# Kernel tuning notes

Measured on AMD Instinct MI355X. Metric: run time of the kernel, lower is better.

The kernel has to match this reference:

```python
import jax, jax.numpy as jnp
import numpy as np

VOCAB = 50000
EMBED = 256
LABELS = 2
DEPTH = 10          # complete binary tree: 2**DEPTH leaves
B = 256             # batch of trees
L = 2 ** DEPTH      # leaves per tree


def setup_inputs() -> dict:
    key = jax.random.key(0)
    ks = jax.random.split(key, 7)
    token_ids = jax.random.randint(ks[0], (B, L), 0, VOCAB)
    labels = jax.random.randint(ks[1], (B,), 0, LABELS)
    emb = jax.random.normal(ks[2], (VOCAB, EMBED), dtype=jnp.float32)
    W_w = jax.random.normal(ks[3], (EMBED, 2 * EMBED), dtype=jnp.float32) * (1.0 / np.sqrt(2 * EMBED))
    W_b = jax.random.normal(ks[4], (EMBED,), dtype=jnp.float32) * 0.01
    P_w = jax.random.normal(ks[5], (LABELS, EMBED), dtype=jnp.float32) * (1.0 / np.sqrt(EMBED))
    P_b = jax.random.normal(ks[6], (LABELS,), dtype=jnp.float32) * 0.01
    return {"token_ids": token_ids, "labels": labels, "emb": emb,
            "W_w": W_w, "W_b": W_b, "P_w": P_w, "P_b": P_b}


def reference(token_ids, labels, emb, W_w, W_b, P_w, P_b):
    # Leaves: relu(embedding(token))  -> [B, L, E]
    x = jax.nn.relu(emb[token_ids])
    # Level-by-level combine: currentNode = relu(W @ cat(left, right) + b)
    # Leaf order is left-to-right, so adjacent pairs (2k, 2k+1) are siblings;
    # reshape concatenates (left, right) along features, matching torch.cat((l, r), 1).
    while x.shape[1] > 1:
        bsz, n, e = x.shape
        lr = x.reshape(bsz, n // 2, 2 * e)                       # [B, n/2, 2E]
        x = jax.nn.relu(jnp.einsum('bnf,ef->bne', lr, W_w) + W_b)
    root = x[:, 0]                                               # [B, E]
    logits = root @ P_w.T + P_b                                  # [B, label_size]
    prediction = jnp.argmax(logits, axis=1)
    logp = jax.nn.log_softmax(logits, axis=-1)
    loss = -jnp.take_along_axis(logp, labels[:, None], axis=1)[:, 0]  # per-tree CE
    return prediction, loss
```

## Files before the change

### kernel.cpp

```cpp
#include <hip/hip_runtime.h>
#include <hip/hip_bf16.h>
#include <math.h>

#define EMBED   256
#define KDIM    512
#define BATCH   256
#define BM      128

typedef float  f32x4   __attribute__((ext_vector_type(4)));
typedef __bf16 bf16x8  __attribute__((ext_vector_type(8)));
typedef unsigned short ushort8 __attribute__((ext_vector_type(8)));

__device__ __forceinline__ unsigned short f2h(float f) {
    unsigned int u = __float_as_uint(f);
    u += 0x7FFFu + ((u >> 16) & 1u);
    return (unsigned short)(u >> 16);
}
__device__ __forceinline__ float h2f(unsigned short h) {
    return __uint_as_float(((unsigned int)h) << 16);
}
__device__ __forceinline__ void gload16(const void* g, void* l) {
    __builtin_amdgcn_global_load_lds(
        (const __attribute__((address_space(1))) unsigned int*)g,
        (__attribute__((address_space(3))) unsigned int*)l, 16, 0, 0);
}

template<int LV1, int WPREP>
__global__ __launch_bounds__(1024, 4) void gemm_tree(
    const unsigned short* __restrict__ Xh, const unsigned short* __restrict__ Xl,
    const unsigned short* __restrict__ Wh, const unsigned short* __restrict__ Wl,
    const float*  __restrict__ Wf,
    const float*  __restrict__ bias,
    unsigned short* __restrict__ Yh, unsigned short* __restrict__ Yl,
    const int* __restrict__ tok, const float* __restrict__ emb)
{
    __shared__ __align__(16) unsigned short AhL[2][4096], AlL[2][4096];
    __shared__ __align__(16) unsigned short BhL[2][8192], BlL[2][8192];

    const int tid = threadIdx.x;
    const int wid = tid >> 6;
    const int l   = tid & 63;
    const int q   = l >> 4;
    const int rr  = l & 15;
    const int m0  = blockIdx.x * BM;
    const int waveM = wid >> 2;
    const int waveN = wid & 3;

    int tokA0 = 0, tokA1 = 0;
    if constexpr (LV1) {
        if (wid < 8) {
            const int r = m0 + wid * 16 + rr;
            tokA0 = tok[2 * r];
            tokA1 = tok[2 * r + 1];
        }
    }

    float va[8];
    float vb[8];

    f32x4 acc[2][4] = {};

    auto stage_issue = [&](int buf, int k0) {
        const int joff = k0 >> 8;
        const int c    = (k0 & 255) + q * 8;
        if constexpr (LV1) {
            if (wid < 8) {
                const int t = joff ? tokA1 : tokA0;
                const float* e = emb + (size_t)t * EMBED + c;
                *(float4*)&va[0] = *(const float4*)e;
                *(float4*)&va[4] = *(const float4*)(e + 4);
            }
            if constexpr (WPREP) {
                #pragma unroll
                for (int j = 0; j < 2; ++j) {
                    const int sb = wid * 2 + j;
                    const int s  = sb & 15;
                    const size_t off = (size_t)(s * 16 + rr) * KDIM + k0 + q * 8;
                    if (sb < 16) gload16(Wh + off, &BhL[buf][s * 512]);
                    else         gload16(Wl + off, &BlL[buf][s * 512]);
                }
            } else {
                const float* ws = Wf + (size_t)(wid * 16 + rr) * KDIM + k0 + q * 8;
                *(float4*)&vb[0] = *(const float4*)ws;
                *(float4*)&vb[4] = *(const float4*)(ws + 4);
            }
        } else {
            if constexpr (WPREP) {
                #pragma unroll
                for (int j = 0; j < 3; ++j) {
                    const int slot = wid * 3 + j;
                    if (slot < 16) {
                        const int s = slot & 7;
                        const size_t off = (size_t)(2 * (m0 + s * 16 + rr) + joff) * EMBED + c;
                        if (slot < 8) gload16(Xh + off, &AhL[buf][s * 512]);
                        else          gload16(Xl + off, &AlL[buf][s * 512]);
                    } else {
                        const int s = slot & 15;
                        const size_t off = (size_t)(s * 16 + rr) * KDIM + k0 + q * 8;
                        if (slot < 32) gload16(Wh + off, &BhL[buf][s * 512]);
                        else           gload16(Wl + off, &BlL[buf][s * 512]);
                    }
                }
            } else {
                const int s = wid & 7;
                const size_t off = (size_t)(2 * (m0 + s * 16 + rr) + joff) * EMBED + c;
                if (wid < 8) gload16(Xh + off, &AhL[buf][s * 512]);
                else         gload16(Xl + off, &AlL[buf][s * 512]);
                const float* ws = Wf + (size_t)(wid * 16 + rr) * KDIM + k0 + q * 8;
                *(float4*)&vb[0] = *(const float4*)ws;
                *(float4*)&vb[4] = *(const float4*)(ws + 4);
            }
        }
    };

    auto stage_finish = [&](int buf) {
        if constexpr (LV1) {
            if (wid < 8) {
                ushort8 hs, ls;
                #pragma unroll
                for (int i = 0; i < 8; ++i) {
                    const float f = fmaxf(va[i], 0.f);
                    const unsigned short h = f2h(f);
                    hs[i] = h;
                    ls[i] = f2h(f - h2f(h));
                }
                *(ushort8*)&AhL[buf][wid * 512 + l * 8] = hs;
                *(ushort8*)&AlL[buf][wid * 512 + l * 8] = ls;
            }
        }
        if constexpr (!WPREP) {
            ushort8 hs, ls;
            #pragma unroll
            for (int i = 0; i < 8; ++i) {
                const unsigned short h = f2h(vb[i]);
                hs[i] = h;
                ls[i] = f2h(vb[i] - h2f(h));
            }
            *(ushort8*)&BhL[buf][wid * 512 + l * 8] = hs;
            *(ushort8*)&BlL[buf][wid * 512 + l * 8] = ls;
        }
    };

    stage_issue(0, 0);
    stage_finish(0);
    __syncthreads();

    for (int t = 0; t < 16; ++t) {
        const int cur = t & 1;
        const int nxt = cur ^ 1;
        if (t < 15) stage_issue(nxt, (t + 1) << 5);

        bf16x8 ah[2], al[2], bh[4], bl[4];
        #pragma unroll
        for (int mi = 0; mi < 2; ++mi) {
            ah[mi] = *(const bf16x8*)&AhL[cur][(waveM * 2 + mi) * 512 + l * 8];
            al[mi] = *(const bf16x8*)&AlL[cur][(waveM * 2 + mi) * 512 + l * 8];
        }
        #pragma unroll
        for (int ni = 0; ni < 4; ++ni) {
            bh[ni] = *(const bf16x8*)&BhL[cur][(waveN * 4 + ni) * 512 + l * 8];
            bl[ni] = *(const bf16x8*)&BlL[cur][(waveN * 4 + ni) * 512 + l * 8];
        }
        #pragma unroll
        for (int mi = 0; mi < 2; ++mi)
            #pragma unroll
            for (int ni = 0; ni < 4; ++ni)
                acc[mi][ni] = __builtin_amdgcn_mfma_f32_16x16x32_bf16(ah[mi], bh[ni], acc[mi][ni], 0, 0, 0);
        #pragma unroll
        for (int mi = 0; mi < 2; ++mi)
            #pragma unroll
            for (int ni = 0; ni < 4; ++ni)
                acc[mi][ni] = __builtin_amdgcn_mfma_f32_16x16x32_bf16(al[mi], bh[ni], acc[mi][ni], 0, 0, 0);
        #pragma unroll
        for (int mi = 0; mi < 2; ++mi)
            #pragma unroll
            for (int ni = 0; ni < 4; ++ni)
                acc[mi][ni] = __builtin_amdgcn_mfma_f32_16x16x32_bf16(ah[mi], bl[ni], acc[mi][ni], 0, 0, 0);

        if (t < 15) stage_finish(nxt);
        __syncthreads();
    }

    #pragma unroll
    for (int ni = 0; ni < 4; ++ni) {
        const int col = waveN * 64 + ni * 16 + rr;
        const float bv = bias[col];
        #pragma unroll
        for (int mi = 0; mi < 2; ++mi) {
            const int row0 = m0 + waveM * 32 + mi * 16 + q * 4;
            #pragma unroll
            for (int jj = 0; jj < 4; ++jj) {
                const float y = fmaxf(acc[mi][ni][jj] + bv, 0.f);
                const unsigned short h = f2h(y);
                Yh[(size_t)(row0 + jj) * EMBED + col] = h;
                Yl[(size_t)(row0 + jj) * EMBED + col] = f2h(y - h2f(h));
            }
        }
    }
}

template<int WPREP>
__global__ __launch_bounds__(256) void tail_kernel(
    const unsigned short* __restrict__ Xh5, const unsigned short* __restrict__ Xl5,
    const unsigned short* __restrict__ Wh, const unsigned short* __restrict__ Wl,
    const float* __restrict__ Wf, const float* __restrict__ bias,
    const float* __restrict__ Pw, const float* __restrict__ Pb,
    const int* __restrict__ labels, float* __restrict__ out)
{
    __shared__ __align__(16) unsigned short X0h[8192], X0l[8192];
    __shared__ __align__(16) unsigned short X1h[4096], X1l[4096];
    __shared__ __align__(16) unsigned short BhT[2][8192], BlT[2][8192];

    const int tid = threadIdx.x;
    const int w   = tid >> 6;
    const int l   = tid & 63;
    const int q   = l >> 4;
    const int rr  = l & 15;
    const int b   = blockIdx.x;

    {
        const int row = tid >> 3;
        const int c0  = (tid & 7) * 32;
        #pragma unroll
        for (int i = 0; i < 4; ++i) {
            const int col = c0 + i * 8;
            const int sw  = (row * 256 + col) ^ ((row & 7) << 3);
            *(ushort8*)&X0h[sw] = *(const ushort8*)&Xh5[(size_t)(b * 32 + row) * EMBED + col];
            *(ushort8*)&X0l[sw] = *(const ushort8*)&Xl5[(size_t)(b * 32 + row) * EMBED + col];
        }
    }

    auto stageB = [&](int buf, int k0) {
        if constexpr (WPREP) {
            #pragma unroll
            for (int j = 0; j < 8; ++j) {
                const int sb = w * 8 + j;
                const int s  = sb & 15;
                const size_t off = (size_t)(s * 16 + rr) * KDIM + k0 + q * 8;
                if (sb < 16) gload16(Wh + off, &BhT[buf][s * 512]);
                else         gload16(Wl + off, &BlT[buf][s * 512]);
            }
        } else {
            #pragma unroll
            for (int j = 0; j < 4; ++j) {
                const int u = w * 4 + j;
                const float* ws = Wf + (size_t)(u * 16 + rr) * KDIM + k0 + q * 8;
                float v[8];
                *(float4*)&v[0] = *(const float4*)ws;
                *(float4*)&v[4] = *(const float4*)(ws + 4);
                ushort8 hs, ls;
                #pragma unroll
                for (int i = 0; i < 8; ++i) {
                    const unsigned short h = f2h(v[i]);
                    hs[i] = h;
                    ls[i] = f2h(v[i] - h2f(h));
                }
                *(ushort8*)&BhT[buf][u * 512 + l * 8] = hs;
                *(ushort8*)&BlT[buf][u * 512 + l * 8] = ls;
            }
        }
    };

    float bv[4];
    #pragma unroll
    for (int ni = 0; ni < 4; ++ni) bv[ni] = bias[w * 64 + ni * 16 + rr];

    stageB(0, 0);
    __syncthreads();

    int g = 0;
    for (int lv = 0; lv < 5; ++lv) {
        unsigned short* srch = (lv & 1) ? X1h : X0h;
        unsigned short* srcl = (lv & 1) ? X1l : X0l;
        unsigned short* dsth = (lv & 1) ? X0h : X1h;
        unsigned short* dstl = (lv & 1) ? X0l : X1l;
        const int Mout = 16 >> lv;

        f32x4 acc[4] = {};
        for (int t = 0; t < 16; ++t, ++g) {
            const int cur = g & 1;
            if (g < 79) stageB(cur ^ 1, ((t + 1) & 15) * 32);

            const int k0   = t * 32;
            const int joff = k0 >> 8;
            const int c    = (k0 & 255) + q * 8;
            const int row  = 2 * rr + joff;
            const int idx  = (row * 256 + c) ^ ((row & 7) << 3);
            const bf16x8 a_h = *(const bf16x8*)&srch[idx];
            const bf16x8 a_l = *(const bf16x8*)&srcl[idx];

            bf16x8 bh4[4], bl4[4];
            #pragma unroll
            for (int ni = 0; ni < 4; ++ni) {
                bh4[ni] = *(const bf16x8*)&BhT[cur][(w * 4 + ni) * 512 + l * 8];
                bl4[ni] = *(const bf16x8*)&BlT[cur][(w * 4 + ni) * 512 + l * 8];
            }
            #pragma unroll
            for (int ni = 0; ni < 4; ++ni)
                acc[ni] = __builtin_amdgcn_mfma_f32_16x16x32_bf16(a_h, bh4[ni], acc[ni], 0, 0, 0);
            #pragma unroll
            for (int ni = 0; ni < 4; ++ni)
                acc[ni] = __builtin_amdgcn_mfma_f32_16x16x32_bf16(a_l, bh4[ni], acc[ni], 0, 0, 0);
            #pragma unroll
            for (int ni = 0; ni < 4; ++ni)
                acc[ni] = __builtin_amdgcn_mfma_f32_16x16x32_bf16(a_h, bl4[ni], acc[ni], 0, 0, 0);

            __syncthreads();
        }

        #pragma unroll
        for (int ni = 0; ni < 4; ++ni) {
            const int col = w * 64 + ni * 16 + rr;
            #pragma unroll
            for (int jj = 0; jj < 4; ++jj) {
                const int row = q * 4 + jj;
                if (row < Mout) {
                    const float y = fmaxf(acc[ni][jj] + bv[ni], 0.f);
                    const unsigned short h = f2h(y);
                    const int idx = (row * 256 + col) ^ ((row & 7) << 3);
                    dsth[idx] = h;
                    dstl[idx] = f2h(y - h2f(h));
                }
            }
        }
        __syncthreads();
    }

    if (w == 0) {
        float s0 = 0.f, s1 = 0.f;
        #pragma unroll
        for (int i = 0; i < 4; ++i) {
            const int col = l + i * 64;
            const float x = h2f(X1h[col]) + h2f(X1l[col]);
            s0 = fmaf(x, Pw[col], s0);
            s1 = fmaf(x, Pw[EMBED + col], s1);
        }
        #pragma unroll
        for (int off = 32; off > 0; off >>= 1) {
            s0 += __shfl_down(s0, off);
            s1 += __shfl_down(s1, off);
        }
        if (l == 0) {
            const float l0 = s0 + Pb[0];
            const float l1 = s1 + Pb[1];
            const int pred = (l1 > l0) ? 1 : 0;
            const float m  = fmaxf(l0, l1);
            const float lse = m + logf(expf(l0 - m) + expf(l1 - m));
            const int lab = labels[b];
            out[b]         = (float)pred;
            out[BATCH + b] = lse - (lab ? l1 : l0);
        }
    }
}

__global__ __launch_bounds__(256) void prep_w(const float* __restrict__ W,
                                              unsigned short* __restrict__ Wh,
                                              unsigned short* __restrict__ Wl)
{
    const int i = blockIdx.x * 256 + threadIdx.x;
    const float w = W[i];
    const unsigned short h = f2h(w);
    Wh[i] = h;
    Wl[i] = f2h(w - h2f(h));
}

extern "C" void kernel_launch(void* const* d_in, const int* in_sizes, int n_in,
                              void* d_out, int out_size, void* d_ws, size_t ws_size,
                              hipStream_t stream)
{
    const int*   token_ids = (const int*)d_in[0];
    const int*   labels    = (const int*)d_in[1];
    const float* emb       = (const float*)d_in[2];
    const float* W_w       = (const float*)d_in[3];
    const float* W_b       = (const float*)d_in[4];
    const float* P_w       = (const float*)d_in[5];
    const float* P_b       = (const float*)d_in[6];
    float*       out       = (float*)d_out;

    unsigned short* Ah_buf = (unsigned short*)d_ws;
    unsigned short* Al_buf = Ah_buf + (size_t)131072 * 256;
    unsigned short* Bh_buf = Al_buf + (size_t)131072 * 256;
    unsigned short* Bl_buf = Bh_buf + (size_t)65536 * 256;
    unsigned short* Wh     = Bl_buf + (size_t)65536 * 256;
    unsigned short* Wl     = Wh + 131072;

    const size_t need_wprep = ((size_t)131072 * 256 * 2 + (size_t)65536 * 256 * 2 + 2 * 131072) * 2;
    const bool wprep = ws_size >= need_wprep;

    if (wprep) prep_w<<<512, 256, 0, stream>>>(W_w, Wh, Wl);

    int R = 131072;
    const unsigned short *inh = nullptr, *inl = nullptr;
    for (int lv = 1; lv <= 5; ++lv) {
        unsigned short* yh = (lv & 1) ? Ah_buf : Bh_buf;
        unsigned short* yl = (lv & 1) ? Al_buf : Bl_buf;
        dim3 grid(R / BM);
        if (lv == 1) {
            if (wprep) gemm_tree<1,1><<<grid, 1024, 0, stream>>>(nullptr, nullptr, Wh, Wl, W_w, W_b, yh, yl, token_ids, emb);
            else       gemm_tree<1,0><<<grid, 1024, 0, stream>>>(nullptr, nullptr, Wh, Wl, W_w, W_b, yh, yl, token_ids, emb);
        } else {
            if (wprep) gemm_tree<0,1><<<grid, 1024, 0, stream>>>(inh, inl, Wh, Wl, W_w, W_b, yh, yl, nullptr, nullptr);
            else       gemm_tree<0,0><<<grid, 1024, 0, stream>>>(inh, inl, Wh, Wl, W_w, W_b, yh, yl, nullptr, nullptr);
        }
        inh = yh; inl = yl; R >>= 1;
    }

    if (wprep) tail_kernel<1><<<BATCH, 256, 0, stream>>>(inh, inl, Wh, Wl, W_w, W_b, P_w, P_b, labels, out);
    else       tail_kernel<0><<<BATCH, 256, 0, stream>>>(inh, inl, Wh, Wl, W_w, W_b, P_w, P_b, labels, out);
}
```

Before: 434.8 us.

## Retile tree GEMM to 128x128 tiles with 4 waves and swizzled grid

Replaces the 1024-thread block computing a 128x256 tile with a 256-thread block computing a 128x128 tile. Each wave now holds a 64x64 accumulator, which raises MFMA work per LDS read. The grid doubles along N and block order is swizzled so tiles sharing an A slab run near each other. The double-buffered prefetch is dropped for a single buffer with two barriers per K step. That lowers LDS use and may raise occupancy, but load latency is no longer hidden behind compute within a block.

```diff
diff --git a/kernel.cpp b/kernel.cpp
--- a/kernel.cpp
+++ b/kernel.cpp
@@ -6,6 +6,7 @@
 #define KDIM    512
 #define BATCH   256
 #define BM      128
+#define BN      128
 
 typedef float  f32x4   __attribute__((ext_vector_type(4)));
 typedef __bf16 bf16x8  __attribute__((ext_vector_type(8)));
@@ -26,7 +27,7 @@
 }
 
 template<int LV1, int WPREP>
-__global__ __launch_bounds__(1024, 4) void gemm_tree(
+__global__ __launch_bounds__(256) void gemm_tree(
     const unsigned short* __restrict__ Xh, const unsigned short* __restrict__ Xl,
     const unsigned short* __restrict__ Wh, const unsigned short* __restrict__ Wl,
     const float*  __restrict__ Wf,
@@ -34,160 +35,137 @@
     unsigned short* __restrict__ Yh, unsigned short* __restrict__ Yl,
     const int* __restrict__ tok, const float* __restrict__ emb)
 {
-    __shared__ __align__(16) unsigned short AhL[2][4096], AlL[2][4096];
-    __shared__ __align__(16) unsigned short BhL[2][8192], BlL[2][8192];
+    __shared__ __align__(16) unsigned short AhL[4096], AlL[4096];
+    __shared__ __align__(16) unsigned short BhL[4096], BlL[4096];
 
     const int tid = threadIdx.x;
-    const int wid = tid >> 6;
+    const int w   = tid >> 6;
     const int l   = tid & 63;
     const int q   = l >> 4;
     const int rr  = l & 15;
-    const int m0  = blockIdx.x * BM;
-    const int waveM = wid >> 2;
-    const int waveN = wid & 3;
-
-    int tokA0 = 0, tokA1 = 0;
+
+    const int nwg = gridDim.x;
+    const int bid = blockIdx.x;
+    const int swz = (bid & 7) * (nwg >> 3) + (bid >> 3);
+    const int m0  = (swz >> 1) * BM;
+    const int n0  = (swz & 1) * BN;
+
+    const int waveM = w >> 1;
+    const int waveN = w & 1;
+
+    int tk[2][2];
     if constexpr (LV1) {
-        if (wid < 8) {
-            const int r = m0 + wid * 16 + rr;
-            tokA0 = tok[2 * r];
-            tokA1 = tok[2 * r + 1];
-        }
-    }
-
-    float va[8];
-    float vb[8];
-
-    f32x4 acc[2][4] = {};
-
-    auto stage_issue = [&](int buf, int k0) {
+        #pragma unroll
+        for (int g = 0; g < 2; ++g) {
+            const int r = m0 + (w + g * 4) * 16 + rr;
+            tk[g][0] = tok[2 * r];
+            tk[g][1] = tok[2 * r + 1];
+        }
+    }
+
+    f32x4 acc[4][4] = {};
+
+    for (int t = 0; t < 16; ++t) {
+        const int k0   = t << 5;
         const int joff = k0 >> 8;
         const int c    = (k0 & 255) + q * 8;
+
         if constexpr (LV1) {
-            if (wid < 8) {
-                const int t = joff ? tokA1 : tokA0;
-                const float* e = emb + (size_t)t * EMBED + c;
-                *(float4*)&va[0] = *(const float4*)e;
-                *(float4*)&va[4] = *(const float4*)(e + 4);
-            }
-            if constexpr (WPREP) {
-                #pragma unroll
-                for (int j = 0; j < 2; ++j) {
-                    const int sb = wid * 2 + j;
-                    const int s  = sb & 15;
-                    const size_t off = (size_t)(s * 16 + rr) * KDIM + k0 + q * 8;
-                    if (sb < 16) gload16(Wh + off, &BhL[buf][s * 512]);
-                    else         gload16(Wl + off, &BlL[buf][s * 512]);
-                }
-            } else {
-                const float* ws = Wf + (size_t)(wid * 16 + rr) * KDIM + k0 + q * 8;
-                *(float4*)&vb[0] = *(const float4*)ws;
-                *(float4*)&vb[4] = *(const float4*)(ws + 4);
-            }
-        } else {
-            if constexpr (WPREP) {
-                #pragma unroll
-                for (int j = 0; j < 3; ++j) {
-                    const int slot = wid * 3 + j;
-                    if (slot < 16) {
-                        const int s = slot & 7;
-                        const size_t off = (size_t)(2 * (m0 + s * 16 + rr) + joff) * EMBED + c;
-                        if (slot < 8) gload16(Xh + off, &AhL[buf][s * 512]);
-                        else          gload16(Xl + off, &AlL[buf][s * 512]);
-                    } else {
-                        const int s = slot & 15;
-                        const size_t off = (size_t)(s * 16 + rr) * KDIM + k0 + q * 8;
-                        if (slot < 32) gload16(Wh + off, &BhL[buf][s * 512]);
-                        else           gload16(Wl + off, &BlL[buf][s * 512]);
-                    }
-                }
-            } else {
-                const int s = wid & 7;
-                const size_t off = (size_t)(2 * (m0 + s * 16 + rr) + joff) * EMBED + c;
-                if (wid < 8) gload16(Xh + off, &AhL[buf][s * 512]);
-                else         gload16(Xl + off, &AlL[buf][s * 512]);
-                const float* ws = Wf + (size_t)(wid * 16 + rr) * KDIM + k0 + q * 8;
-                *(float4*)&vb[0] = *(const float4*)ws;
-                *(float4*)&vb[4] = *(const float4*)(ws + 4);
-            }
-        }
-    };
-
-    auto stage_finish = [&](int buf) {
-        if constexpr (LV1) {
-            if (wid < 8) {
+            #pragma unroll
+            for (int g = 0; g < 2; ++g) {
+                const int s = w + g * 4;
+                const float* e = emb + (size_t)tk[g][joff] * EMBED + c;
+                float v[8];
+                *(float4*)&v[0] = *(const float4*)e;
+                *(float4*)&v[4] = *(const float4*)(e + 4);
                 ushort8 hs, ls;
                 #pragma unroll
                 for (int i = 0; i < 8; ++i) {
-                    const float f = fmaxf(va[i], 0.f);
+                    const float f = fmaxf(v[i], 0.f);
                     const unsigned short h = f2h(f);
                     hs[i] = h;
                     ls[i] = f2h(f - h2f(h));
                 }
-                *(ushort8*)&AhL[buf][wid * 512 + l * 8] = hs;
-                *(ushort8*)&AlL[buf][wid * 512 + l * 8] = ls;
-            }
-        }
-        if constexpr (!WPREP) {
-            ushort8 hs, ls;
-            #pragma unroll
-            for (int i = 0; i < 8; ++i) {
-                const unsigned short h = f2h(vb[i]);
-                hs[i] = h;
-                ls[i] = f2h(vb[i] - h2f(h));
-            }
-            *(ushort8*)&BhL[buf][wid * 512 + l * 8] = hs;
-            *(ushort8*)&BlL[buf][wid * 512 + l * 8] = ls;
-        }
-    };
-
-    stage_issue(0, 0);
-    stage_finish(0);
-    __syncthreads();
-
-    for (int t = 0; t < 16; ++t) {
-        const int cur = t & 1;
-        const int nxt = cur ^ 1;
-        if (t < 15) stage_issue(nxt, (t + 1) << 5);
-
-        bf16x8 ah[2], al[2], bh[4], bl[4];
-        #pragma unroll
-        for (int mi = 0; mi < 2; ++mi) {
-            ah[mi] = *(const bf16x8*)&AhL[cur][(waveM * 2 + mi) * 512 + l * 8];
-            al[mi] = *(const bf16x8*)&AlL[cur][(waveM * 2 + mi) * 512 + l * 8];
-        }
-        #pragma unroll
-        for (int ni = 0; ni < 4; ++ni) {
-            bh[ni] = *(const bf16x8*)&BhL[cur][(waveN * 4 + ni) * 512 + l * 8];
-            bl[ni] = *(const bf16x8*)&BlL[cur][(waveN * 4 + ni) * 512 + l * 8];
-        }
-        #pragma unroll
-        for (int mi = 0; mi < 2; ++mi)
-            #pragma unroll
-            for (int ni = 0; ni < 4; ++ni)
-                acc[mi][ni] = __builtin_amdgcn_mfma_f32_16x16x32_bf16(ah[mi], bh[ni], acc[mi][ni], 0, 0, 0);
-        #pragma unroll
-        for (int mi = 0; mi < 2; ++mi)
-            #pragma unroll
-            for (int ni = 0; ni < 4; ++ni)
-                acc[mi][ni] = __builtin_amdgcn_mfma_f32_16x16x32_bf16(al[mi], bh[ni], acc[mi][ni], 0, 0, 0);
-        #pragma unroll
-        for (int mi = 0; mi < 2; ++mi)
-            #pragma unroll
-            for (int ni = 0; ni < 4; ++ni)
-                acc[mi][ni] = __builtin_amdgcn_mfma_f32_16x16x32_bf16(ah[mi], bl[ni], acc[mi][ni], 0, 0, 0);
-
-        if (t < 15) stage_finish(nxt);
+                *(ushort8*)&AhL[s * 512 + l * 8] = hs;
+                *(ushort8*)&AlL[s * 512 + l * 8] = ls;
+            }
+        } else {
+            #pragma unroll
+            for (int g = 0; g < 2; ++g) {
+                const int s = w + g * 4;
+                const size_t off = (size_t)(2 * (m0 + s * 16 + rr) + joff) * EMBED + c;
+                gload16(Xh + off, &AhL[s * 512]);
+                gload16(Xl + off, &AlL[s * 512]);
+            }
+        }
+
+        #pragma unroll
+        for (int g = 0; g < 2; ++g) {
+            const int s = w + g * 4;
+            if constexpr (WPREP) {
+                const size_t off = (size_t)(n0 + s * 16 + rr) * KDIM + k0 + q * 8;
+                gload16(Wh + off, &BhL[s * 512]);
+                gload16(Wl + off, &BlL[s * 512]);
+            } else {
+                const float* ws = Wf + (size_t)(n0 + s * 16 + rr) * KDIM + k0 + q * 8;
+                float v[8];
+                *(float4*)&v[0] = *(const float4*)ws;
+                *(float4*)&v[4] = *(const float4*)(ws + 4);
+                ushort8 hs, ls;
+                #pragma unroll
+                for (int i = 0; i < 8; ++i) {
+                    const unsigned short h = f2h(v[i]);
+                    hs[i] = h;
+                    ls[i] = f2h(v[i] - h2f(h));
+                }
+                *(ushort8*)&BhL[s * 512 + l * 8] = hs;
+                *(ushort8*)&BlL[s * 512 + l * 8] = ls;
+            }
+        }
+
+        __syncthreads();
+
+        bf16x8 a0[4], b0[4], x0[4];
+        #pragma unroll
+        for (int mi = 0; mi < 4; ++mi)
+            a0[mi] = *(const bf16x8*)&AhL[(waveM * 4 + mi) * 512 + l * 8];
+        #pragma unroll
+        for (int ni = 0; ni < 4; ++ni)
+            b0[ni] = *(const bf16x8*)&BhL[(waveN * 4 + ni) * 512 + l * 8];
+        #pragma unroll
+        for (int mi = 0; mi < 4; ++mi)
+            #pragma unroll
+            for (int ni = 0; ni < 4; ++ni)
+                acc[mi][ni] = __builtin_amdgcn_mfma_f32_16x16x32_bf16(a0[mi], b0[ni], acc[mi][ni], 0, 0, 0);
+
+        #pragma unroll
+        for (int ni = 0; ni < 4; ++ni)
+            x0[ni] = *(const bf16x8*)&BlL[(waveN * 4 + ni) * 512 + l * 8];
+        #pragma unroll
+        for (int mi = 0; mi < 4; ++mi)
+            #pragma unroll
+            for (int ni = 0; ni < 4; ++ni)
+                acc[mi][ni] = __builtin_amdgcn_mfma_f32_16x16x32_bf16(a0[mi], x0[ni], acc[mi][ni], 0, 0, 0);
+
+        #pragma unroll
+        for (int mi = 0; mi < 4; ++mi)
+            x0[mi] = *(const bf16x8*)&AlL[(waveM * 4 + mi) * 512 + l * 8];
+        #pragma unroll
+        for (int mi = 0; mi < 4; ++mi)
+            #pragma unroll
+            for (int ni = 0; ni < 4; ++ni)
+                acc[mi][ni] = __builtin_amdgcn_mfma_f32_16x16x32_bf16(x0[mi], b0[ni], acc[mi][ni], 0, 0, 0);
+
         __syncthreads();
     }
 
     #pragma unroll
     for (int ni = 0; ni < 4; ++ni) {
-        const int col = waveN * 64 + ni * 16 + rr;
+        const int col = n0 + waveN * 64 + ni * 16 + rr;
         const float bv = bias[col];
         #pragma unroll
-        for (int mi = 0; mi < 2; ++mi) {
-            const int row0 = m0 + waveM * 32 + mi * 16 + q * 4;
+        for (int mi = 0; mi < 4; ++mi) {
+            const int row0 = m0 + waveM * 64 + mi * 16 + q * 4;
             #pragma unroll
             for (int jj = 0; jj < 4; ++jj) {
                 const float y = fmaxf(acc[mi][ni][jj] + bv, 0.f);
@@ -394,13 +372,13 @@
     for (int lv = 1; lv <= 5; ++lv) {
         unsigned short* yh = (lv & 1) ? Ah_buf : Bh_buf;
         unsigned short* yl = (lv & 1) ? Al_buf : Bl_buf;
-        dim3 grid(R / BM);
+        dim3 grid((R / BM) * 2);
         if (lv == 1) {
-            if (wprep) gemm_tree<1,1><<<grid, 1024, 0, stream>>>(nullptr, nullptr, Wh, Wl, W_w, W_b, yh, yl, token_ids, emb);
-            else       gemm_tree<1,0><<<grid, 1024, 0, stream>>>(nullptr, nullptr, Wh, Wl, W_w, W_b, yh, yl, token_ids, emb);
+            if (wprep) gemm_tree<1,1><<<grid, 256, 0, stream>>>(nullptr, nullptr, Wh, Wl, W_w, W_b, yh, yl, token_ids, emb);
+            else       gemm_tree<1,0><<<grid, 256, 0, stream>>>(nullptr, nullptr, Wh, Wl, W_w, W_b, yh, yl, token_ids, emb);
         } else {
-            if (wprep) gemm_tree<0,1><<<grid, 1024, 0, stream>>>(inh, inl, Wh, Wl, W_w, W_b, yh, yl, nullptr, nullptr);
-            else       gemm_tree<0,0><<<grid, 1024, 0, stream>>>(inh, inl, Wh, Wl, W_w, W_b, yh, yl, nullptr, nullptr);
+            if (wprep) gemm_tree<0,1><<<grid, 256, 0, stream>>>(inh, inl, Wh, Wl, W_w, W_b, yh, yl, nullptr, nullptr);
+            else       gemm_tree<0,0><<<grid, 256, 0, stream>>>(inh, inl, Wh, Wl, W_w, W_b, yh, yl, nullptr, nullptr);
         }
         inh = yh; inl = yl; R >>= 1;
     }
```

New measurement: 449.6 us. 3.4% more time.
